# Kernel tuning notes

Hardware: AMD Instinct MI355X
Metric: run time of the kernel (lower is better)

## Reference

```python
import jax, jax.numpy as jnp
import numpy as np

KP_VARIANCE = 0.01  # init kwarg: kp_variance (float -> plain Gaussian branch)


def make_coordinate_grid(h, w, dtype):
    # torch make_coordinate_grid: x,y in [-1,1], last dim is (x, y)
    x = jnp.linspace(-1.0, 1.0, w, dtype=dtype)
    y = jnp.linspace(-1.0, 1.0, h, dtype=dtype)
    gx, gy = jnp.meshgrid(x, y)  # each (h, w)
    return jnp.stack([gx, gy], axis=-1)  # (h, w, 2)


def grid_sample_bilinear(img, coords):
    """F.grid_sample, bilinear, zeros padding, align_corners=True.
    img: (bs, C, H, W); coords: (bs, d, K, h, w, 2) with (x, y) in [-1,1].
    Returns (bs, d, K, C, h, w)."""
    bs, C, H, W = img.shape
    x = (coords[..., 0] + 1.0) * (W - 1) / 2.0
    y = (coords[..., 1] + 1.0) * (H - 1) / 2.0
    x0 = jnp.floor(x); y0 = jnp.floor(y)
    x1 = x0 + 1.0;     y1 = y0 + 1.0
    wx1 = x - x0; wx0 = 1.0 - wx1
    wy1 = y - y0; wy0 = 1.0 - wy1

    def corner(ix, iy, wgt):
        valid = (ix >= 0) & (ix <= W - 1) & (iy >= 0) & (iy <= H - 1)
        ixc = jnp.clip(ix, 0, W - 1).astype(jnp.int32)
        iyc = jnp.clip(iy, 0, H - 1).astype(jnp.int32)
        # per-batch gather: im (C,H,W), yy/xx (d,K,h,w) -> (C,d,K,h,w)
        vals = jax.vmap(lambda im, yy, xx: im[:, yy, xx])(img, iyc, ixc)  # (bs,C,d,K,h,w)
        w_eff = (wgt * valid.astype(img.dtype))[:, None]  # (bs,1,d,K,h,w)
        return vals * w_eff

    out = (corner(x0, y0, wx0 * wy0) + corner(x1, y0, wx1 * wy0)
           + corner(x0, y1, wx0 * wy1) + corner(x1, y1, wx1 * wy1))
    return jnp.transpose(out, (0, 2, 3, 1, 4, 5))  # (bs,d,K,C,h,w)


def setup_inputs() -> dict:
    key = jax.random.key(0)
    k1, k2, k3 = jax.random.split(key, 3)
    bs, d, K, C, h, w = 4, 16, 10, 3, 128, 128
    kp_appearance_mean = jax.random.uniform(k1, (bs, 1, K, 2), jnp.float32) * 2.0 - 1.0
    kp_video_mean = jax.random.uniform(k2, (bs, d, K, 2), jnp.float32) * 2.0 - 1.0
    appearance_frame = jax.random.normal(k3, (bs, C, 1, h, w), jnp.float32)
    return {"kp_appearance_mean": kp_appearance_mean,
            "kp_video_mean": kp_video_mean,
            "appearance_frame": appearance_frame}


def reference(kp_appearance_mean, kp_video_mean, appearance_frame):
    bs, C, _, h, w = appearance_frame.shape
    _, d, K, _ = kp_video_mean.shape
    dtype = appearance_frame.dtype

    # combine_kp (difference_type='absolute', float kp_variance)
    diff = kp_video_mean - kp_video_mean[:, 0:1]          # (bs,d,K,2)
    kp_mean = diff + kp_appearance_mean                    # (bs,d,K,2)
    kp_video_diff = -diff                                  # (bs,d,K,2)

    grid = make_coordinate_grid(h, w, dtype)               # (h,w,2)

    # use_heatmap: kp2gaussian then subtract first frame
    mean_sub = grid - kp_mean[:, :, :, None, None, :]      # (bs,d,K,h,w,2)
    heatmap = jnp.exp(-0.5 * jnp.sum(mean_sub * mean_sub, axis=-1) / KP_VARIANCE)
    heatmap = heatmap - heatmap[:, 0:1]
    heatmap = heatmap[:, :, :, None]                       # (bs,d,K,1,h,w)

    # use_difference: broadcast diff over spatial dims
    diff_maps = jnp.broadcast_to(kp_video_diff[:, :, :, :, None, None],
                                 (bs, d, K, 2, h, w))

    # use_deformed_appearance: grid_sample of appearance frame by shifted grid
    deformation = grid + kp_video_diff[:, :, :, None, None, :]  # (bs,d,K,h,w,2)
    img = appearance_frame[:, :, 0]                              # (bs,C,h,w)
    deformed = grid_sample_bilinear(img, deformation)            # (bs,d,K,C,h,w)

    enc = jnp.concatenate([heatmap, diff_maps, deformed], axis=3)  # (bs,d,K,1+2+C,h,w)
    enc = enc.reshape(bs, d, -1, h, w)
    return jnp.transpose(enc, (0, 2, 1, 3, 4))  # (bs, (3+C)*K, d, h, w)
```

## Files before the change

### kernel.cpp

```cpp
#include <hip/hip_runtime.h>

#define BS 4
#define DD 16
#define KK 10
#define CC 3
#define HH 128
#define WW 128

__global__ __launch_bounds__(256) void movement_embed_kernel(
    const float* __restrict__ kp_app,
    const float* __restrict__ kp_vid,
    const float* __restrict__ img,
    float* __restrict__ out)
{
    const unsigned bi  = blockIdx.x;
    const unsigned sub = bi & 15u;
    const unsigned bdk = bi >> 4;
    const unsigned k   = bdk % KK;
    const unsigned t2  = bdk / KK;
    const unsigned d   = t2 % DD;
    const unsigned b   = t2 / DD;

    const unsigned p  = sub * 256u + threadIdx.x;
    const unsigned xg = p & 31u;
    const unsigned y  = p >> 5;

    const float kvx  = kp_vid[((b*DD + d)*KK + k)*2 + 0];
    const float kvy  = kp_vid[((b*DD + d)*KK + k)*2 + 1];
    const float kv0x = kp_vid[((b*DD + 0)*KK + k)*2 + 0];
    const float kv0y = kp_vid[((b*DD + 0)*KK + k)*2 + 1];
    const float kax  = kp_app[(b*KK + k)*2 + 0];
    const float kay  = kp_app[(b*KK + k)*2 + 1];

    const float diffx = kvx - kv0x;
    const float diffy = kvy - kv0y;
    const float mx = diffx + kax;
    const float my = diffy + kay;
    const float vdx = -diffx;
    const float vdy = -diffy;

    const float step = 2.0f / 127.0f;
    const float gy = (float)y * step - 1.0f;

    const float yi  = (gy + vdy + 1.0f) * 63.5f;
    const float y0f = floorf(yi);
    const float fy  = yi - y0f;
    const int   y0  = (int)y0f;
    const int   y1  = y0 + 1;
    const float wy0 = (1.0f - fy) * ((y0 >= 0 && y0 < HH) ? 1.0f : 0.0f);
    const float wy1 = fy          * ((y1 >= 0 && y1 < HH) ? 1.0f : 0.0f);
    const int   y0c = min(max(y0, 0), HH - 1);
    const int   y1c = min(max(y1, 0), HH - 1);

    const float dy1 = gy - my;
    const float dy0 = gy - kay;
    const float dy1sq = dy1 * dy1;
    const float dy0sq = dy0 * dy0;

    const float* imgb = img + (size_t)b * CC * HH * WW;

    float hv[4];
    float dv[CC][4];

#pragma unroll
    for (int j = 0; j < 4; ++j) {
        const int   x  = (int)(xg * 4u) + j;
        const float gx = (float)x * step - 1.0f;

        const float dx1 = gx - mx;
        const float dx0 = gx - kax;
        const float e1 = __expf(-50.0f * (dx1 * dx1 + dy1sq));
        const float e0 = __expf(-50.0f * (dx0 * dx0 + dy0sq));
        hv[j] = e1 - e0;

        const float xi  = (gx + vdx + 1.0f) * 63.5f;
        const float x0f = floorf(xi);
        const float fx  = xi - x0f;
        const int   x0  = (int)x0f;
        const int   x1  = x0 + 1;
        const float wx0 = (1.0f - fx) * ((x0 >= 0 && x0 < WW) ? 1.0f : 0.0f);
        const float wx1 = fx          * ((x1 >= 0 && x1 < WW) ? 1.0f : 0.0f);
        const int   x0c = min(max(x0, 0), WW - 1);
        const int   x1c = min(max(x1, 0), WW - 1);

        const float w00 = wx0 * wy0, w10 = wx1 * wy0;
        const float w01 = wx0 * wy1, w11 = wx1 * wy1;

#pragma unroll
        for (int c = 0; c < CC; ++c) {
            const float* pc = imgb + (size_t)c * HH * WW;
            const float* r0 = pc + (size_t)y0c * WW;
            const float* r1 = pc + (size_t)y1c * WW;
            dv[c][j] = w00 * r0[x0c] + w10 * r0[x1c]
                     + w01 * r1[x0c] + w11 * r1[x1c];
        }
    }

    const size_t chs  = (size_t)DD * HH * WW;
    const size_t base = ((((size_t)b * (KK * 6) + k * 6) * DD + d) * HH + y) * WW + xg * 4u;

    *(float4*)(out + base)           = make_float4(hv[0], hv[1], hv[2], hv[3]);
    *(float4*)(out + base + chs)     = make_float4(vdx, vdx, vdx, vdx);
    *(float4*)(out + base + 2*chs)   = make_float4(vdy, vdy, vdy, vdy);
#pragma unroll
    for (int c = 0; c < CC; ++c) {
        *(float4*)(out + base + (size_t)(3 + c) * chs) =
            make_float4(dv[c][0], dv[c][1], dv[c][2], dv[c][3]);
    }
}

extern "C" void kernel_launch(void* const* d_in, const int* in_sizes, int n_in,
                              void* d_out, int out_size, void* d_ws, size_t ws_size,
                              hipStream_t stream) {
    const float* kp_app = (const float*)d_in[0];
    const float* kp_vid = (const float*)d_in[1];
    const float* img    = (const float*)d_in[2];
    float* out = (float*)d_out;

    const int nblocks = BS * DD * KK * 16;
    movement_embed_kernel<<<nblocks, 256, 0, stream>>>(kp_app, kp_vid, img, out);
}
```

Baseline: 294.2 us.

## Stage shifted image patch in LDS and exploit uniform translation for bilinear sampling

```diff
diff --git a/kernel.cpp b/kernel.cpp
--- a/kernel.cpp
+++ b/kernel.cpp
@@ -7,12 +7,17 @@
 #define HH 128
 #define WW 128
 
+#define NROWS 9
+#define LROW 132
+
 __global__ __launch_bounds__(256) void movement_embed_kernel(
     const float* __restrict__ kp_app,
     const float* __restrict__ kp_vid,
     const float* __restrict__ img,
     float* __restrict__ out)
 {
+    __shared__ __align__(16) float P[CC][NROWS][LROW];
+
     const unsigned bi  = blockIdx.x;
     const unsigned sub = bi & 15u;
     const unsigned bdk = bi >> 4;
@@ -20,10 +25,7 @@
     const unsigned t2  = bdk / KK;
     const unsigned d   = t2 % DD;
     const unsigned b   = t2 / DD;
-
-    const unsigned p  = sub * 256u + threadIdx.x;
-    const unsigned xg = p & 31u;
-    const unsigned y  = p >> 5;
+    const int tid = (int)threadIdx.x;
 
     const float kvx  = kp_vid[((b*DD + d)*KK + k)*2 + 0];
     const float kvy  = kp_vid[((b*DD + d)*KK + k)*2 + 1];
@@ -39,74 +41,84 @@
     const float vdx = -diffx;
     const float vdy = -diffy;
 
+    const float cx = vdx * 63.5f;
+    const float cy = vdy * 63.5f;
+    const float fcx = floorf(cx);
+    const float fcy = floorf(cy);
+    const int icx = (int)fcx;
+    const int icy = (int)fcy;
+    const float wx1 = cx - fcx, wx0 = 1.0f - wx1;
+    const float wy1 = cy - fcy, wy0 = 1.0f - wy1;
+
+    const int R0 = (int)(sub * 8u) + icy;
+    const float* imgb = img + (size_t)b * (CC*HH*WW);
+
+    for (int idx = tid; idx < CC*NROWS*129; idx += 256) {
+        const int tt    = idx % 129;
+        const int rowix = idx / 129;
+        const int ri = rowix % NROWS;
+        const int c  = rowix / NROWS;
+        const int r   = R0 + ri;
+        const int col = icx + tt;
+        float v = 0.0f;
+        if ((unsigned)r < (unsigned)HH && (unsigned)col < (unsigned)WW)
+            v = imgb[(c*HH + r)*WW + col];
+        P[c][ri][tt] = v;
+    }
+    __syncthreads();
+
+    const int xg = tid & 31;
+    const int ly = tid >> 5;
+    const int x4 = xg * 4;
+    const int y  = (int)(sub * 8u) + ly;
+
     const float step = 2.0f / 127.0f;
-    const float gy = (float)y * step - 1.0f;
+    const float gy  = (float)y  * step - 1.0f;
+    const float gx0 = (float)x4 * step - 1.0f;
 
-    const float yi  = (gy + vdy + 1.0f) * 63.5f;
-    const float y0f = floorf(yi);
-    const float fy  = yi - y0f;
-    const int   y0  = (int)y0f;
-    const int   y1  = y0 + 1;
-    const float wy0 = (1.0f - fy) * ((y0 >= 0 && y0 < HH) ? 1.0f : 0.0f);
-    const float wy1 = fy          * ((y1 >= 0 && y1 < HH) ? 1.0f : 0.0f);
-    const int   y0c = min(max(y0, 0), HH - 1);
-    const int   y1c = min(max(y1, 0), HH - 1);
-
-    const float dy1 = gy - my;
-    const float dy0 = gy - kay;
-    const float dy1sq = dy1 * dy1;
-    const float dy0sq = dy0 * dy0;
-
-    const float* imgb = img + (size_t)b * CC * HH * WW;
-
+    const float dy1 = gy - my, dy0 = gy - kay;
+    const float dy1sq = dy1 * dy1, dy0sq = dy0 * dy0;
     float hv[4];
-    float dv[CC][4];
-
 #pragma unroll
     for (int j = 0; j < 4; ++j) {
-        const int   x  = (int)(xg * 4u) + j;
-        const float gx = (float)x * step - 1.0f;
+        const float gx = gx0 + (float)j * step;
+        const float dx1 = gx - mx, dx0 = gx - kax;
+        hv[j] = __expf(-50.0f * (dx1 * dx1 + dy1sq))
+              - __expf(-50.0f * (dx0 * dx0 + dy0sq));
+    }
 
-        const float dx1 = gx - mx;
-        const float dx0 = gx - kax;
-        const float e1 = __expf(-50.0f * (dx1 * dx1 + dy1sq));
-        const float e0 = __expf(-50.0f * (dx0 * dx0 + dy0sq));
-        hv[j] = e1 - e0;
-
-        const float xi  = (gx + vdx + 1.0f) * 63.5f;
-        const float x0f = floorf(xi);
-        const float fx  = xi - x0f;
-        const int   x0  = (int)x0f;
-        const int   x1  = x0 + 1;
-        const float wx0 = (1.0f - fx) * ((x0 >= 0 && x0 < WW) ? 1.0f : 0.0f);
-        const float wx1 = fx          * ((x1 >= 0 && x1 < WW) ? 1.0f : 0.0f);
-        const int   x0c = min(max(x0, 0), WW - 1);
-        const int   x1c = min(max(x1, 0), WW - 1);
-
-        const float w00 = wx0 * wy0, w10 = wx1 * wy0;
-        const float w01 = wx0 * wy1, w11 = wx1 * wy1;
-
+    float4 dvc[CC];
 #pragma unroll
-        for (int c = 0; c < CC; ++c) {
-            const float* pc = imgb + (size_t)c * HH * WW;
-            const float* r0 = pc + (size_t)y0c * WW;
-            const float* r1 = pc + (size_t)y1c * WW;
-            dv[c][j] = w00 * r0[x0c] + w10 * r0[x1c]
-                     + w01 * r1[x0c] + w11 * r1[x1c];
-        }
+    for (int c = 0; c < CC; ++c) {
+        const float* row0 = &P[c][ly][x4];
+        const float* row1 = &P[c][ly + 1][x4];
+        const float4 A = *(const float4*)row0;
+        const float  ea = row0[4];
+        const float4 B = *(const float4*)row1;
+        const float  eb = row1[4];
+        const float h0x = wx0 * A.x + wx1 * A.y;
+        const float h0y = wx0 * A.y + wx1 * A.z;
+        const float h0z = wx0 * A.z + wx1 * A.w;
+        const float h0w = wx0 * A.w + wx1 * ea;
+        const float h1x = wx0 * B.x + wx1 * B.y;
+        const float h1y = wx0 * B.y + wx1 * B.z;
+        const float h1z = wx0 * B.z + wx1 * B.w;
+        const float h1w = wx0 * B.w + wx1 * eb;
+        dvc[c] = make_float4(wy0 * h0x + wy1 * h1x,
+                             wy0 * h0y + wy1 * h1y,
+                             wy0 * h0z + wy1 * h1z,
+                             wy0 * h0w + wy1 * h1w);
     }
 
     const size_t chs  = (size_t)DD * HH * WW;
-    const size_t base = ((((size_t)b * (KK * 6) + k * 6) * DD + d) * HH + y) * WW + xg * 4u;
+    const size_t base = ((((size_t)b * (KK * 6) + k * 6) * DD + d) * HH + y) * WW + (size_t)x4;
 
-    *(float4*)(out + base)           = make_float4(hv[0], hv[1], hv[2], hv[3]);
-    *(float4*)(out + base + chs)     = make_float4(vdx, vdx, vdx, vdx);
-    *(float4*)(out + base + 2*chs)   = make_float4(vdy, vdy, vdy, vdy);
+    *(float4*)(out + base)         = make_float4(hv[0], hv[1], hv[2], hv[3]);
+    *(float4*)(out + base + chs)   = make_float4(vdx, vdx, vdx, vdx);
+    *(float4*)(out + base + 2*chs) = make_float4(vdy, vdy, vdy, vdy);
 #pragma unroll
-    for (int c = 0; c < CC; ++c) {
-        *(float4*)(out + base + (size_t)(3 + c) * chs) =
-            make_float4(dv[c][0], dv[c][1], dv[c][2], dv[c][3]);
-    }
+    for (int c = 0; c < CC; ++c)
+        *(float4*)(out + base + (size_t)(3 + c) * chs) = dvc[c];
 }
 
 extern "C" void kernel_launch(void* const* d_in, const int* in_sizes, int n_in,
```

Result: faster. 254.6 us (-13.5%).
